# Kernel tuning notes

Measured on AMD Instinct MI355X. Metric: run time of the kernel, lower is better.

The kernel has to match this reference:

```python
import jax, jax.numpy as jnp
import numpy as np

B, C, H, W = 256, 3, 128, 128
IN_DIM = C * 2 * H * W  # 98304
H1, H2, OUT = 512, 256, 128


def _freq_features(x):
    # x: [3, 128, 128] -> [3*2*128*128] features (amp, phase per channel)
    f = jnp.fft.fftshift(jnp.fft.fft2(x), axes=(-2, -1))
    amp = jnp.abs(f)
    ph = jnp.angle(f)
    # order matches original: [amp_c0, ph_c0, amp_c1, ph_c1, amp_c2, ph_c2]
    return jnp.stack([amp, ph], axis=1).reshape(-1).astype(jnp.float32)


def setup_inputs() -> dict:
    key = jax.random.key(0)
    ks = jax.random.split(key, 7)
    img = jax.random.normal(ks[0], (B, C, H, W), dtype=jnp.float32)
    s1 = 1.0 / np.sqrt(IN_DIM)
    s2 = 1.0 / np.sqrt(H1)
    s3 = 1.0 / np.sqrt(H2)
    W1 = jax.random.uniform(ks[1], (H1, IN_DIM), jnp.float32, -s1, s1)
    b1 = jax.random.uniform(ks[2], (H1,), jnp.float32, -s1, s1)
    W2 = jax.random.uniform(ks[3], (H2, H1), jnp.float32, -s2, s2)
    b2 = jax.random.uniform(ks[4], (H2,), jnp.float32, -s2, s2)
    W3 = jax.random.uniform(ks[5], (OUT, H2), jnp.float32, -s3, s3)
    b3 = jax.random.uniform(ks[6], (OUT,), jnp.float32, -s3, s3)
    return {"img": img, "W1": W1, "b1": b1, "W2": W2, "b2": b2, "W3": W3, "b3": b3}


def reference(img, W1, b1, W2, b2, W3, b3):
    feats = jax.vmap(_freq_features)(img)  # [B, 98304]
    x = jax.nn.relu(feats @ W1.T + b1)
    x = jax.nn.relu(x @ W2.T + b2)
    return x @ W3.T + b3  # [B, 128]
```

## Files before the change

### kernel.cpp

```cpp
#include <hip/hip_runtime.h>
#include <hip/hip_bf16.h>

#define IN_DIM 98304

typedef short bh8 __attribute__((ext_vector_type(8)));
typedef float f32x4 __attribute__((ext_vector_type(4)));
typedef unsigned short u16x8 __attribute__((ext_vector_type(8)));

__device__ __forceinline__ unsigned short f2bf(float f) {
  __hip_bfloat16 h = __float2bfloat16(f);
  return __builtin_bit_cast(unsigned short, h);
}

__device__ __forceinline__ void gload_lds16(const void* g, void* l) {
  __builtin_amdgcn_global_load_lds(
      (const __attribute__((address_space(1))) void*)g,
      (__attribute__((address_space(3))) void*)l, 16, 0, 0);
}

__device__ __forceinline__ void bfly(float2& a, float2& b, float wr, float wi) {
  float tr = wr * b.x - wi * b.y;
  float ti = wr * b.y + wi * b.x;
  b.x = a.x - tr; b.y = a.y - ti;
  a.x += tr; a.y += ti;
}

__device__ __forceinline__ float2 cmul(float2 a, float2 w) {
  return make_float2(a.x * w.x - a.y * w.y, a.x * w.y + a.y * w.x);
}

__device__ __forceinline__ void fft16(float2* v) {
  const float C8 = 0.70710678118654752f;
  const float C161 = 0.92387953251128674f, S161 = 0.38268343236508977f;
#pragma unroll
  for (int i = 0; i < 16; i += 2) bfly(v[i], v[i + 1], 1.f, 0.f);
#pragma unroll
  for (int i = 0; i < 16; i += 4) {
    bfly(v[i], v[i + 2], 1.f, 0.f);
    bfly(v[i + 1], v[i + 3], 0.f, -1.f);
  }
  {
    const float w8r[4] = {1.f, C8, 0.f, -C8};
    const float w8i[4] = {0.f, -C8, -1.f, -C8};
#pragma unroll
    for (int i = 0; i < 16; i += 8) {
#pragma unroll
      for (int j = 0; j < 4; ++j) bfly(v[i + j], v[i + j + 4], w8r[j], w8i[j]);
    }
  }
  {
    const float w16r[8] = {1.f, C161, C8, S161, 0.f, -S161, -C8, -C161};
    const float w16i[8] = {0.f, -S161, -C8, -C161, -1.f, -C161, -C8, -S161};
#pragma unroll
    for (int j = 0; j < 8; ++j) bfly(v[j], v[j + 8], w16r[j], w16i[j]);
  }
}

__device__ __forceinline__ void fft8(float2* v) {
  const float C8 = 0.70710678118654752f;
#pragma unroll
  for (int i = 0; i < 8; i += 2) bfly(v[i], v[i + 1], 1.f, 0.f);
#pragma unroll
  for (int i = 0; i < 8; i += 4) {
    bfly(v[i], v[i + 2], 1.f, 0.f);
    bfly(v[i + 1], v[i + 3], 0.f, -1.f);
  }
  bfly(v[0], v[4], 1.f, 0.f);
  bfly(v[1], v[5], C8, -C8);
  bfly(v[2], v[6], 0.f, -1.f);
  bfly(v[3], v[7], -C8, -C8);
}

__device__ __forceinline__ int TIX(int r, int cc) {
  return (r << 6) + (cc ^ ((r & 7) << 1));
}

__global__ __launch_bounds__(512, 4) void fft_feats_kernel(
    const float* __restrict__ img, unsigned short* __restrict__ feats) {
  __shared__ float2 tile[128 * 64];
  __shared__ float2 sm64[128];
  __shared__ float2 tw[128];
  const int tid = threadIdx.x;
  const int ch = blockIdx.x, b = blockIdx.y;
  const float* src = img + ((size_t)(b * 3 + ch) << 14);

  static const int BR4[16] = {0, 8, 4, 12, 2, 10, 6, 14, 1, 9, 5, 13, 3, 11, 7, 15};
  static const int BR3[8] = {0, 4, 2, 6, 1, 5, 3, 7};

  if (tid < 128) {
    float sv, cv;
    sincosf(-6.28318530717958647692f * (float)tid / 128.0f, &sv, &cv);
    tw[tid] = make_float2(cv, sv);
  }
#pragma unroll
  for (int it = 0; it < 8; ++it) {
    int i4 = it * 512 + tid;
    int r = i4 >> 5, c4 = i4 & 31;
    float4 x = *reinterpret_cast<const float4*>(src + (i4 << 2));
    *reinterpret_cast<float4*>(&tile[TIX(r, c4 * 2)]) = x;
  }
  __syncthreads();

#pragma unroll
  for (int it = 0; it < 2; ++it) {
    int g = it * 512 + tid;
    int r = g >> 3, n2 = g & 7;
    float2 v[8];
#pragma unroll
    for (int j = 0; j < 8; ++j) v[j] = tile[TIX(r, (BR3[j] << 3) + n2)];
    fft8(v);
#pragma unroll
    for (int k1 = 1; k1 < 8; ++k1) v[k1] = cmul(v[k1], tw[2 * n2 * k1]);
#pragma unroll
    for (int k1 = 0; k1 < 8; ++k1) tile[TIX(r, (k1 << 3) + n2)] = v[k1];
  }
  __syncthreads();

  {
    int r0 = tid >> 3, t8 = tid & 7;
    int r1 = r0 + 64;
    float2 ua[8], ub[8];
#pragma unroll
    for (int j = 0; j < 8; ++j) {
      ua[j] = tile[TIX(r0, (t8 << 3) + BR3[j])];
      ub[j] = tile[TIX(r1, (t8 << 3) + BR3[j])];
    }
    __syncthreads();
    fft8(ua);
    fft8(ub);
#pragma unroll
    for (int k2 = 0; k2 < 8; ++k2) {
      tile[TIX(r0, t8 + (k2 << 3))] = ua[k2];
      tile[TIX(r1, t8 + (k2 << 3))] = ub[k2];
    }
  }
  __syncthreads();

#pragma unroll
  for (int it = 0; it < 8; ++it) {
    int g = it * 512 + tid;
    int r = g >> 5, k = g & 31;
    if (k == 0) {
      float2 z0 = tile[TIX(r, 0)];
      float2 z32 = tile[TIX(r, 32)];
      tile[TIX(r, 0)] = make_float2(z0.x + z0.y, 0.f);
      sm64[r] = make_float2(z0.x - z0.y, 0.f);
      tile[TIX(r, 32)] = make_float2(z32.x, -z32.y);
    } else {
      float2 zk = tile[TIX(r, k)];
      float2 zm = tile[TIX(r, 64 - k)];
      float2 ze = make_float2(0.5f * (zk.x + zm.x), 0.5f * (zk.y - zm.y));
      float2 zo = make_float2(0.5f * (zk.y + zm.y), -0.5f * (zk.x - zm.x));
      float2 t = cmul(zo, tw[k]);
      tile[TIX(r, k)] = make_float2(ze.x + t.x, ze.y + t.y);
      tile[TIX(r, 64 - k)] = make_float2(ze.x - t.x, -(ze.y - t.y));
    }
  }
  __syncthreads();

  {
    int col = tid & 63, n2 = tid >> 6;
    float2 v[16];
#pragma unroll
    for (int j = 0; j < 16; ++j) v[j] = tile[TIX((BR4[j] << 3) + n2, col)];
    fft16(v);
#pragma unroll
    for (int k1 = 1; k1 < 16; ++k1) v[k1] = cmul(v[k1], tw[n2 * k1]);
#pragma unroll
    for (int k1 = 0; k1 < 16; ++k1) tile[TIX((k1 << 3) + n2, col)] = v[k1];
    if (tid < 8) {
      int m2 = tid;
      float2 w[16];
#pragma unroll
      for (int j = 0; j < 16; ++j) w[j] = sm64[(BR4[j] << 3) + m2];
      fft16(w);
#pragma unroll
      for (int k1 = 1; k1 < 16; ++k1) w[k1] = cmul(w[k1], tw[m2 * k1]);
#pragma unroll
      for (int k1 = 0; k1 < 16; ++k1) sm64[(k1 << 3) + m2] = w[k1];
    }
  }
  __syncthreads();

  unsigned short* dst = feats + (size_t)b * IN_DIM + ch * 32768;
  {
    int col = tid & 63, t8 = tid >> 6;
    float2 u0[8], u1[8];
#pragma unroll
    for (int j = 0; j < 8; ++j) {
      u0[j] = tile[TIX((t8 << 3) + BR3[j], col)];
      u1[j] = tile[TIX(((t8 + 8) << 3) + BR3[j], col)];
    }
    fft8(u0);
    fft8(u1);
    const int ow = col + 64;
    const int owm = 64 - col;
#pragma unroll
    for (int k2 = 0; k2 < 8; ++k2) {
#pragma unroll
      for (int half = 0; half < 2; ++half) {
        float2 F = half ? u1[k2] : u0[k2];
        int kh = t8 + half * 8 + (k2 << 4);
        float amp = sqrtf(F.x * F.x + F.y * F.y);
        float ph = atan2f(F.y, F.x);
        int oh = kh ^ 64;
        dst[(oh << 7) + ow] = f2bf(amp);
        dst[16384 + (oh << 7) + ow] = f2bf(ph);
        if (col != 0) {
          int khm = (128 - kh) & 127;
          int ohm = khm ^ 64;
          dst[(ohm << 7) + owm] = f2bf(amp);
          dst[16384 + (ohm << 7) + owm] = f2bf(-ph);
        }
      }
    }
    if (tid < 8) {
      int t8t = tid;
      float2 e0[8], e1[8];
#pragma unroll
      for (int j = 0; j < 8; ++j) {
        e0[j] = sm64[(t8t << 3) + BR3[j]];
        e1[j] = sm64[((t8t + 8) << 3) + BR3[j]];
      }
      fft8(e0);
      fft8(e1);
#pragma unroll
      for (int k2 = 0; k2 < 8; ++k2) {
#pragma unroll
        for (int half = 0; half < 2; ++half) {
          float2 F = half ? e1[k2] : e0[k2];
          int kh = t8t + half * 8 + (k2 << 4);
          float amp = sqrtf(F.x * F.x + F.y * F.y);
          float ph = atan2f(F.y, F.x);
          int oh = kh ^ 64;
          dst[(oh << 7)] = f2bf(amp);
          dst[16384 + (oh << 7)] = f2bf(ph);
        }
      }
    }
  }
}

#define GS 64
#define GITERS 48

__global__ __launch_bounds__(512, 2) void gemm1_kernel(
    const unsigned short* __restrict__ feats, const float* __restrict__ W1,
    float* __restrict__ partial) {
  __shared__ __align__(16) unsigned short Asm[4][256 * 32];
  __shared__ __align__(16) unsigned short Bsm[2][128 * 32];
  const int tid = threadIdx.x;
  const int wv = tid >> 6, lane = tid & 63;

  const int f = blockIdx.x;
  const int xcd = f & 7, v = f >> 3;
  const int ks = xcd * 8 + (v & 7);
  const int nt = v >> 3;
  const int n0 = nt * 128;
  const size_t k0 = (size_t)ks * (GITERS * 32);

  const int al_row = lane >> 2;
  const int al_k = (lane & 3) * 8;
  const int brow = tid >> 2, bq = tid & 3;
  const float* bsrc = W1 + (size_t)(n0 + brow) * IN_DIM + k0 + bq * 8;

  auto stageA = [&](int buf, int it) {
    const size_t kb = k0 + (size_t)it * 32;
#pragma unroll
    for (int tl = 0; tl < 2; ++tl) {
      const int s = wv * 2 + tl;
      const unsigned short* ga =
          feats + (size_t)(s * 16 + al_row) * IN_DIM + kb + al_k;
      gload_lds16(ga, (char*)&Asm[buf][0] + s * 1024);
    }
  };

  float4 br0, br1;
  auto loadB = [&](int it) {
    const float* p = bsrc + (size_t)it * 32;
    br0 = *reinterpret_cast<const float4*>(p);
    br1 = *reinterpret_cast<const float4*>(p + 4);
  };
  auto writeB = [&](int buf) {
    u16x8 bw;
    bw[0] = f2bf(br0.x); bw[1] = f2bf(br0.y); bw[2] = f2bf(br0.z); bw[3] = f2bf(br0.w);
    bw[4] = f2bf(br1.x); bw[5] = f2bf(br1.y); bw[6] = f2bf(br1.z); bw[7] = f2bf(br1.w);
    *reinterpret_cast<u16x8*>(&Bsm[buf][brow * 32 + bq * 8]) = bw;
  };

  f32x4 acc[4][4];
#pragma unroll
  for (int i = 0; i < 4; ++i)
#pragma unroll
    for (int jj = 0; jj < 4; ++jj) acc[i][jj] = (f32x4){0.f, 0.f, 0.f, 0.f};

  const int mr = wv & 3;
  const int nc = wv >> 2;
  const int rm = lane & 15, hi = lane >> 4;

  stageA(0, 0);
  stageA(1, 1);
  stageA(2, 2);
  loadB(0);
  asm volatile("s_waitcnt vmcnt(0)" ::: "memory");
  writeB(0);
  loadB(1);

  for (int k = 0; k < GITERS; ++k) {
    const int rem = GITERS - 1 - k;
    if (rem >= 1) {
      asm volatile("s_waitcnt vmcnt(4) lgkmcnt(0)" ::: "memory");
    } else {
      asm volatile("s_waitcnt vmcnt(0) lgkmcnt(0)" ::: "memory");
    }
    __builtin_amdgcn_sched_barrier(0);
    __builtin_amdgcn_s_barrier();
    __builtin_amdgcn_sched_barrier(0);

    const int abuf = k & 3, bbuf = k & 1;
    bh8 afr[4], bfr[4];
#pragma unroll
    for (int i = 0; i < 4; ++i) {
      const int row = mr * 64 + i * 16 + rm;
      afr[i] = *reinterpret_cast<const bh8*>(&Asm[abuf][row * 32 + hi * 8]);
    }
#pragma unroll
    for (int jj = 0; jj < 4; ++jj) {
      const int row = nc * 64 + jj * 16 + rm;
      bfr[jj] = *reinterpret_cast<const bh8*>(&Bsm[bbuf][row * 32 + hi * 8]);
    }
    __builtin_amdgcn_sched_barrier(0);

    if (rem >= 3) stageA((k + 3) & 3, k + 3);

    if (rem >= 1) {
      if (rem >= 3) {
        asm volatile("s_waitcnt vmcnt(2)" ::: "memory");
      } else {
        asm volatile("s_waitcnt vmcnt(0)" ::: "memory");
      }
      __builtin_amdgcn_sched_barrier(0);
      writeB((k + 1) & 1);
      if (rem >= 2) loadB(k + 2);
    }

    asm volatile("s_waitcnt lgkmcnt(1)" ::: "memory");
    __builtin_amdgcn_sched_barrier(0);

#pragma unroll
    for (int i = 0; i < 4; ++i)
#pragma unroll
      for (int jj = 0; jj < 4; ++jj)
        acc[i][jj] = __builtin_amdgcn_mfma_f32_16x16x32_bf16(
            afr[i], bfr[jj], acc[i][jj], 0, 0, 0);
  }

  const int rg = lane >> 4;
  float* pbase = partial + ((size_t)ks << 17);
#pragma unroll
  for (int i = 0; i < 4; ++i) {
#pragma unroll
    for (int jj = 0; jj < 4; ++jj) {
      const int n = n0 + nc * 64 + jj * 16 + rm;
#pragma unroll
      for (int r = 0; r < 4; ++r) {
        const int m = mr * 64 + i * 16 + rg * 4 + r;
        pbase[((size_t)m << 9) + n] = acc[i][jj][r];
      }
    }
  }
}

__global__ __launch_bounds__(256) void tail_kernel(
    const float* __restrict__ partial, const float* __restrict__ b1,
    const float* __restrict__ W2, const float* __restrict__ b2,
    const float* __restrict__ W3, const float* __restrict__ b3,
    float* __restrict__ out) {
  __shared__ float x1s[512];
  __shared__ float x2s[256];
  const int b = blockIdx.x, n = threadIdx.x;

  {
    float s0 = b1[n], s1 = b1[n + 256];
    const float* pb = partial + ((size_t)b << 9);
#pragma unroll 8
    for (int p = 0; p < GS; ++p) {
      const float* pp = pb + ((size_t)p << 17);
      s0 += pp[n];
      s1 += pp[n + 256];
    }
    x1s[n] = fmaxf(s0, 0.f);
    x1s[n + 256] = fmaxf(s1, 0.f);
  }
  __syncthreads();

  {
    float acc = b2[n];
    const float* wr = W2 + (size_t)n * 512;
#pragma unroll 4
    for (int k = 0; k < 512; k += 4) {
      float4 w = *reinterpret_cast<const float4*>(wr + k);
      acc += x1s[k] * w.x + x1s[k + 1] * w.y + x1s[k + 2] * w.z + x1s[k + 3] * w.w;
    }
    x2s[n] = fmaxf(acc, 0.f);
  }
  __syncthreads();

  if (n < 128) {
    float acc = b3[n];
    const float* wr = W3 + (size_t)n * 256;
#pragma unroll 4
    for (int k = 0; k < 256; k += 4) {
      float4 w = *reinterpret_cast<const float4*>(wr + k);
      acc += x2s[k] * w.x + x2s[k + 1] * w.y + x2s[k + 2] * w.z + x2s[k + 3] * w.w;
    }
    out[b * 128 + n] = acc;
  }
}

extern "C" void kernel_launch(void* const* d_in, const int* in_sizes, int n_in,
                              void* d_out, int out_size, void* d_ws, size_t ws_size,
                              hipStream_t stream) {
  const float* img = (const float*)d_in[0];
  const float* W1 = (const float*)d_in[1];
  const float* b1 = (const float*)d_in[2];
  const float* W2 = (const float*)d_in[3];
  const float* b2 = (const float*)d_in[4];
  const float* W3 = (const float*)d_in[5];
  const float* b3 = (const float*)d_in[6];
  float* out = (float*)d_out;
  char* ws = (char*)d_ws;

  const size_t FEATS_B = 50331648ull;
  unsigned short* feats = (unsigned short*)ws;
  float* partial = (float*)(ws + FEATS_B);

  hipLaunchKernelGGL(fft_feats_kernel, dim3(3, 256), dim3(512), 0, stream, img, feats);
  hipLaunchKernelGGL(gemm1_kernel, dim3(256), dim3(512), 0, stream, feats, W1, partial);
  hipLaunchKernelGGL(tail_kernel, dim3(256), dim3(256), 0, stream,
                     partial, b1, W2, b2, W3, b3, out);
}
```

Before: 138.0 us.

## Double the K-step per iteration in gemm1 and use a 3-stage A ring buffer

The gemm1 main loop now processes 64 K-elements per iteration (two 32-wide halves) instead of 32, halving the number of barriers and wait points per block. The A staging changes from a 4-deep ring of 32-wide tiles to a 3-deep ring of 64-wide tiles, and B is double-buffered with both halves. The larger LDS footprint forces launch bounds down to one block per CU, which trades occupancy for fewer synchronisations and more MFMA work between waits. Waitcnt thresholds are adjusted to the doubled number of outstanding loads.

```diff
diff --git a/kernel.cpp b/kernel.cpp
--- a/kernel.cpp
+++ b/kernel.cpp
@@ -242,13 +242,13 @@
 }
 
 #define GS 64
-#define GITERS 48
-
-__global__ __launch_bounds__(512, 2) void gemm1_kernel(
+#define GIT2 24
+
+__global__ __launch_bounds__(512, 1) void gemm1_kernel(
     const unsigned short* __restrict__ feats, const float* __restrict__ W1,
     float* __restrict__ partial) {
-  __shared__ __align__(16) unsigned short Asm[4][256 * 32];
-  __shared__ __align__(16) unsigned short Bsm[2][128 * 32];
+  __shared__ __align__(16) unsigned short Asm[3][2][256 * 32];
+  __shared__ __align__(16) unsigned short Bsm[2][2][128 * 32];
   const int tid = threadIdx.x;
   const int wv = tid >> 6, lane = tid & 63;
 
@@ -257,7 +257,7 @@
   const int ks = xcd * 8 + (v & 7);
   const int nt = v >> 3;
   const int n0 = nt * 128;
-  const size_t k0 = (size_t)ks * (GITERS * 32);
+  const size_t k0 = (size_t)ks * 1536;
 
   const int al_row = lane >> 2;
   const int al_k = (lane & 3) * 8;
@@ -265,27 +265,38 @@
   const float* bsrc = W1 + (size_t)(n0 + brow) * IN_DIM + k0 + bq * 8;
 
   auto stageA = [&](int buf, int it) {
-    const size_t kb = k0 + (size_t)it * 32;
-#pragma unroll
-    for (int tl = 0; tl < 2; ++tl) {
-      const int s = wv * 2 + tl;
-      const unsigned short* ga =
-          feats + (size_t)(s * 16 + al_row) * IN_DIM + kb + al_k;
-      gload_lds16(ga, (char*)&Asm[buf][0] + s * 1024);
+    const size_t kb = k0 + (size_t)it * 64;
+#pragma unroll
+    for (int h = 0; h < 2; ++h) {
+#pragma unroll
+      for (int tl = 0; tl < 2; ++tl) {
+        const int s = wv * 2 + tl;
+        const unsigned short* ga =
+            feats + (size_t)(s * 16 + al_row) * IN_DIM + kb + h * 32 + al_k;
+        gload_lds16(ga, (char*)&Asm[buf][h][0] + s * 1024);
+      }
     }
   };
 
-  float4 br0, br1;
+  float4 br[2][2];
   auto loadB = [&](int it) {
-    const float* p = bsrc + (size_t)it * 32;
-    br0 = *reinterpret_cast<const float4*>(p);
-    br1 = *reinterpret_cast<const float4*>(p + 4);
+#pragma unroll
+    for (int h = 0; h < 2; ++h) {
+      const float* p = bsrc + (size_t)it * 64 + h * 32;
+      br[h][0] = *reinterpret_cast<const float4*>(p);
+      br[h][1] = *reinterpret_cast<const float4*>(p + 4);
+    }
   };
   auto writeB = [&](int buf) {
-    u16x8 bw;
-    bw[0] = f2bf(br0.x); bw[1] = f2bf(br0.y); bw[2] = f2bf(br0.z); bw[3] = f2bf(br0.w);
-    bw[4] = f2bf(br1.x); bw[5] = f2bf(br1.y); bw[6] = f2bf(br1.z); bw[7] = f2bf(br1.w);
-    *reinterpret_cast<u16x8*>(&Bsm[buf][brow * 32 + bq * 8]) = bw;
+#pragma unroll
+    for (int h = 0; h < 2; ++h) {
+      u16x8 bw;
+      bw[0] = f2bf(br[h][0].x); bw[1] = f2bf(br[h][0].y);
+      bw[2] = f2bf(br[h][0].z); bw[3] = f2bf(br[h][0].w);
+      bw[4] = f2bf(br[h][1].x); bw[5] = f2bf(br[h][1].y);
+      bw[6] = f2bf(br[h][1].z); bw[7] = f2bf(br[h][1].w);
+      *reinterpret_cast<u16x8*>(&Bsm[buf][h][brow * 32 + bq * 8]) = bw;
+    }
   };
 
   f32x4 acc[4][4];
@@ -300,16 +311,16 @@
 
   stageA(0, 0);
   stageA(1, 1);
-  stageA(2, 2);
   loadB(0);
   asm volatile("s_waitcnt vmcnt(0)" ::: "memory");
   writeB(0);
   loadB(1);
 
-  for (int k = 0; k < GITERS; ++k) {
-    const int rem = GITERS - 1 - k;
+  int abuf = 0;
+  for (int k = 0; k < GIT2; ++k) {
+    const int rem = GIT2 - 1 - k;
     if (rem >= 1) {
-      asm volatile("s_waitcnt vmcnt(4) lgkmcnt(0)" ::: "memory");
+      asm volatile("s_waitcnt vmcnt(8) lgkmcnt(0)" ::: "memory");
     } else {
       asm volatile("s_waitcnt vmcnt(0) lgkmcnt(0)" ::: "memory");
     }
@@ -317,25 +328,34 @@
     __builtin_amdgcn_s_barrier();
     __builtin_amdgcn_sched_barrier(0);
 
-    const int abuf = k & 3, bbuf = k & 1;
-    bh8 afr[4], bfr[4];
-#pragma unroll
-    for (int i = 0; i < 4; ++i) {
-      const int row = mr * 64 + i * 16 + rm;
-      afr[i] = *reinterpret_cast<const bh8*>(&Asm[abuf][row * 32 + hi * 8]);
-    }
-#pragma unroll
-    for (int jj = 0; jj < 4; ++jj) {
-      const int row = nc * 64 + jj * 16 + rm;
-      bfr[jj] = *reinterpret_cast<const bh8*>(&Bsm[bbuf][row * 32 + hi * 8]);
+    const int bbuf = k & 1;
+    bh8 afr[2][4], bfr[2][4];
+#pragma unroll
+    for (int h = 0; h < 2; ++h) {
+#pragma unroll
+      for (int i = 0; i < 4; ++i) {
+        const int row = mr * 64 + i * 16 + rm;
+        afr[h][i] =
+            *reinterpret_cast<const bh8*>(&Asm[abuf][h][row * 32 + hi * 8]);
+      }
+#pragma unroll
+      for (int jj = 0; jj < 4; ++jj) {
+        const int row = nc * 64 + jj * 16 + rm;
+        bfr[h][jj] =
+            *reinterpret_cast<const bh8*>(&Bsm[bbuf][h][row * 32 + hi * 8]);
+      }
     }
     __builtin_amdgcn_sched_barrier(0);
 
-    if (rem >= 3) stageA((k + 3) & 3, k + 3);
+    if (rem >= 2) {
+      int sbuf = abuf + 2;
+      if (sbuf >= 3) sbuf -= 3;
+      stageA(sbuf, k + 2);
+    }
 
     if (rem >= 1) {
-      if (rem >= 3) {
-        asm volatile("s_waitcnt vmcnt(2)" ::: "memory");
+      if (rem >= 2) {
+        asm volatile("s_waitcnt vmcnt(4)" ::: "memory");
       } else {
         asm volatile("s_waitcnt vmcnt(0)" ::: "memory");
       }
@@ -344,15 +364,19 @@
       if (rem >= 2) loadB(k + 2);
     }
 
-    asm volatile("s_waitcnt lgkmcnt(1)" ::: "memory");
+    asm volatile("s_waitcnt lgkmcnt(2)" ::: "memory");
     __builtin_amdgcn_sched_barrier(0);
 
 #pragma unroll
-    for (int i = 0; i < 4; ++i)
-#pragma unroll
-      for (int jj = 0; jj < 4; ++jj)
-        acc[i][jj] = __builtin_amdgcn_mfma_f32_16x16x32_bf16(
-            afr[i], bfr[jj], acc[i][jj], 0, 0, 0);
+    for (int h = 0; h < 2; ++h)
+#pragma unroll
+      for (int i = 0; i < 4; ++i)
+#pragma unroll
+        for (int jj = 0; jj < 4; ++jj)
+          acc[i][jj] = __builtin_amdgcn_mfma_f32_16x16x32_bf16(
+              afr[h][i], bfr[h][jj], acc[i][jj], 0, 0, 0);
+
+    abuf = (abuf == 2) ? 0 : abuf + 1;
   }
 
   const int rg = lane >> 4;
```

Measured after the change: 131.8 us (median of 2 runs). 4.5% less time.
